# Kernel tuning notes

Hardware: AMD Instinct MI355X
Metric: run time of the kernel (lower is better)

## Reference

```python
import jax, jax.numpy as jnp
import numpy as np

B = 512
V = 6890   # SMPL vertices
NJ = 24    # joints (global)
NB = 10    # shape betas
NP = 207   # pose blendshape features = 23*9
NJO = 19   # cocoplus output joints
PARENTS = np.array([0,0,0,0,1,2,3,4,5,6,7,8,9,9,9,12,13,14,16,17,18,19,20,21], dtype=np.int32)


def setup_inputs() -> dict:
    key = jax.random.key(0)
    ks = jax.random.split(key, 7)
    inputs = jax.random.normal(ks[0], (B, 82), jnp.float32) * 0.2  # [pose(72) | shape(10)]
    v_template = jax.random.normal(ks[1], (V, 3), jnp.float32)
    shapes = jax.random.normal(ks[2], (NB, V * 3), jnp.float32) * 0.01
    posedirs = jax.random.normal(ks[3], (NP, V * 3), jnp.float32) * 0.01
    jr = jax.random.uniform(ks[4], (V, NJ), jnp.float32)
    smpl_regressor = jr / jnp.sum(jr, axis=0, keepdims=True)          # columns sum to 1 over vertices
    w = jax.random.uniform(ks[5], (V, NJ), jnp.float32) ** 4
    lbs_weights = w / jnp.sum(w, axis=1, keepdims=True)               # rows sum to 1 over joints
    cr = jax.random.uniform(ks[6], (V, NJO), jnp.float32)
    joint_regressor = cr / jnp.sum(cr, axis=0, keepdims=True)
    parents = jnp.asarray(PARENTS)
    return {"inputs": inputs, "v_template": v_template, "shapes": shapes,
            "posedirs": posedirs, "smpl_regressor": smpl_regressor,
            "lbs_weights": lbs_weights, "joint_regressor": joint_regressor,
            "parents": parents}


def _rodrigues(pose):  # [B,72] -> [B,24,3,3]
    r = pose.reshape(-1, 3)
    angle = jnp.linalg.norm(r + 1e-8, axis=1, keepdims=True)  # [N,1]
    n = r / angle
    c = jnp.cos(angle)[:, :, None]   # [N,1,1]
    s = jnp.sin(angle)[:, :, None]
    outer = n[:, :, None] * n[:, None, :]
    z = jnp.zeros_like(n[:, 0])
    K = jnp.stack([z, -n[:, 2], n[:, 1],
                   n[:, 2], z, -n[:, 0],
                   -n[:, 1], n[:, 0], z], axis=1).reshape(-1, 3, 3)
    R = c * jnp.eye(3, dtype=pose.dtype) + (1.0 - c) * outer + s * K
    return R.reshape(-1, NJ, 3, 3)


def _make_A(R, t):  # R [B,3,3], t [B,3] -> [B,4,4]
    top = jnp.concatenate([R, t[:, :, None]], axis=2)
    bottom = jnp.broadcast_to(jnp.array([0., 0., 0., 1.], dtype=R.dtype), (R.shape[0], 1, 4))
    return jnp.concatenate([top, bottom], axis=1)


def _global_rigid(rotations, joints, parents_np):
    # sequential kinematic-chain composition over the fixed 24-joint tree
    res = [_make_A(rotations[:, 0], joints[:, 0])]
    for i in range(1, NJ):
        p = int(parents_np[i])
        t = joints[:, i] - joints[:, p]
        res.append(jnp.matmul(res[p], _make_A(rotations[:, i], t)))
    A_world = jnp.stack(res, axis=1)                 # [B,24,4,4]
    new_J = A_world[:, :, :3, 3]
    Jw0 = jnp.concatenate([joints, jnp.zeros(joints.shape[:2] + (1,), joints.dtype)], axis=2)[..., None]
    init_bone = jnp.matmul(A_world, Jw0)[..., 0]     # [B,24,4]
    pad = jnp.zeros_like(A_world).at[:, :, :, 3].set(init_bone)
    return new_J, A_world - pad


def reference(inputs, v_template, shapes, posedirs, smpl_regressor, lbs_weights, joint_regressor, parents):
    b = inputs.shape[0]
    pose = inputs[:, :72]
    beta = inputs[:, -10:]
    v_shaped = jnp.matmul(beta, shapes).reshape(b, V, 3) + v_template
    v_joints = jnp.einsum('bvc,vj->bjc', v_shaped, smpl_regressor)        # [B,24,3]
    rot = _rodrigues(pose)                                                # [B,24,3,3]
    pose_feature = (rot[:, 1:] - jnp.eye(3, dtype=rot.dtype)).reshape(b, -1)  # [B,207]
    v_posed = jnp.matmul(pose_feature, posedirs).reshape(b, V, 3) + v_shaped
    joint_transformed, A = _global_rigid(rot, v_joints, np.asarray(parents))
    T = jnp.einsum('vj,bjk->bvk', lbs_weights, A.reshape(b, NJ, 16)).reshape(b, V, 4, 4)
    v_homo = jnp.concatenate([v_posed, jnp.ones((b, V, 1), v_posed.dtype)], axis=2)
    vertices = jnp.einsum('bvij,bvj->bvi', T, v_homo)[:, :, :3]
    joints = jnp.einsum('bvc,vj->bjc', vertices, joint_regressor)         # [B,19,3]
    return vertices, joints, rot
```

## Files before the change

kernel.cpp:

```cpp
#include <hip/hip_runtime.h>

#define B_   512
#define V_   6890
#define NJ_  24
#define NB_  10
#define NP_  207
#define NJO_ 19



#define SRB_   192
#define SRCH_  862
#define RODB_  48
#define TRB_   26

__global__ void __launch_bounds__(256) k_pre(const float* __restrict__ in,
                                             const float* __restrict__ shapes,
                                             const float* __restrict__ vt,
                                             const float* __restrict__ sreg,
                                             const float* __restrict__ jreg,
                                             float* __restrict__ srtr,
                                             float* __restrict__ out_rot,
                                             float* __restrict__ pf_t,
                                             float* __restrict__ jreg_t,
                                             float* __restrict__ jout) {
  int blk = blockIdx.x;
  int tid = threadIdx.x;
  if (blk < SRB_) {
    int j  = blk >> 3;
    int ch = blk & 7;
    int vend = (ch + 1) * SRCH_; if (vend > V_) vend = V_;
    float acc[33];
#pragma unroll
    for (int a = 0; a < 33; a++) acc[a] = 0.f;
    for (int v = ch * SRCH_ + tid; v < vend; v += 256) {
      float w = sreg[v * NJ_ + j];
#pragma unroll
      for (int k = 0; k < NB_; k++) {
        const float* sp = shapes + k * (V_ * 3) + 3 * v;
#pragma unroll
        for (int c = 0; c < 3; c++) acc[k * 3 + c] += w * sp[c];
      }
#pragma unroll
      for (int c = 0; c < 3; c++) acc[30 + c] += w * vt[3 * v + c];
    }
    __shared__ float red[4][33];
    int wave = tid >> 6, lane = tid & 63;
#pragma unroll
    for (int a = 0; a < 33; a++) {
      float x = acc[a];
#pragma unroll
      for (int m = 1; m < 64; m <<= 1) x += __shfl_xor(x, m, 64);
      if (lane == 0) red[wave][a] = x;
    }
    __syncthreads();
    if (tid < 33) {
      float s = red[0][tid] + red[1][tid] + red[2][tid] + red[3][tid];
      if (tid < 30) atomicAdd(&srtr[((tid / 3) * NJ_ + j) * 3 + (tid % 3)], s);
      else          atomicAdd(&srtr[720 + j * 3 + (tid - 30)], s);
    }
  } else if (blk < SRB_ + RODB_) {
    int idx = (blk - SRB_) * 256 + tid;
    int b = idx & (B_ - 1);
    int j = idx >> 9;
    const float* r = in + b * 82 + j * 3;
    float r0 = r[0], r1 = r[1], r2 = r[2];
    float ax = r0 + 1e-8f, ay = r1 + 1e-8f, az = r2 + 1e-8f;
    float angle = sqrtf(ax * ax + ay * ay + az * az);
    float inv = 1.0f / angle;
    float n0 = r0 * inv, n1 = r1 * inv, n2 = r2 * inv;
    float c = cosf(angle), s = sinf(angle);
    float ic = 1.0f - c;
    float R[9];
    R[0] = c + ic * n0 * n0;      R[1] = ic * n0 * n1 - s * n2;  R[2] = ic * n0 * n2 + s * n1;
    R[3] = ic * n1 * n0 + s * n2; R[4] = c + ic * n1 * n1;       R[5] = ic * n1 * n2 - s * n0;
    R[6] = ic * n2 * n0 - s * n1; R[7] = ic * n2 * n1 + s * n0;  R[8] = c + ic * n2 * n2;
    float* ro = out_rot + b * 216 + j * 9;
#pragma unroll
    for (int q = 0; q < 9; q++) ro[q] = R[q];
    if (j > 0) {
#pragma unroll
      for (int q = 0; q < 9; q++)
        pf_t[(size_t)((j - 1) * 9 + q) * B_ + b] = R[q] - ((q % 4 == 0) ? 1.0f : 0.0f);
    }
  } else {
    int idx = (blk - SRB_ - RODB_) * 256 + tid;
    for (int q = idx; q < B_ * NJO_ * 3; q += TRB_ * 256) jout[q] = 0.f;
    if (idx < B_) pf_t[(size_t)NP_ * B_ + idx] = 0.f;
    for (int e = idx; e < V_ * NJO_; e += TRB_ * 256) {
      int jo = e / V_;
      int v  = e - jo * V_;
      jreg_t[e] = jreg[v * NJO_ + jo];
    }
  }
}

__global__ void __launch_bounds__(192) k_chain(const float* __restrict__ in,
                                               const float* __restrict__ rot,
                                               const float* __restrict__ srtr,
                                               const int* __restrict__ parents,
                                               float* __restrict__ Abuf) {
  (void)parents;
  constexpr int P[NJ_] = {0, 0, 0, 0, 1, 2, 3, 4, 5, 6, 7, 8, 9, 9, 9, 12, 13, 14,
                          16, 17, 18, 19, 20, 21};
  int tid = threadIdx.x;
  int bl = tid & 63;
  int r  = tid >> 6;
  int b  = blockIdx.x * 64 + bl;
  float beta[NB_];
#pragma unroll
  for (int k = 0; k < NB_; k++) beta[k] = in[b * 82 + 72 + k];
  float J[NJ_][3];
#pragma unroll
  for (int j = 0; j < NJ_; j++) {
#pragma unroll
    for (int c = 0; c < 3; c++) {
      float s = srtr[720 + j * 3 + c];
#pragma unroll
      for (int k = 0; k < NB_; k++) s += beta[k] * srtr[(k * NJ_ + j) * 3 + c];
      J[j][c] = s;
    }
  }
  const float* Rb = rot + b * 216;
  float A[NJ_][4];
#pragma unroll
  for (int c = 0; c < 3; c++) A[0][c] = Rb[r * 3 + c];
  A[0][3] = J[0][r];
#pragma unroll
  for (int j = 1; j < NJ_; j++) {
    const int p = P[j];
    float t0 = J[j][0] - J[p][0];
    float t1 = J[j][1] - J[p][1];
    float t2 = J[j][2] - J[p][2];
    float Rj[9];
#pragma unroll
    for (int q = 0; q < 9; q++) Rj[q] = Rb[j * 9 + q];
    float p0 = A[p][0], p1 = A[p][1], p2 = A[p][2], p3 = A[p][3];
#pragma unroll
    for (int c = 0; c < 3; c++)
      A[j][c] = p0 * Rj[c] + p1 * Rj[3 + c] + p2 * Rj[6 + c];
    A[j][3] = p0 * t0 + p1 * t1 + p2 * t2 + p3;
  }
  float* Ab = Abuf + (size_t)b * 288 + r * 4;
#pragma unroll
  for (int j = 0; j < NJ_; j++) {
    float4 o;
    o.x = A[j][0]; o.y = A[j][1]; o.z = A[j][2];
    o.w = A[j][3] - (A[j][0] * J[j][0] + A[j][1] * J[j][1] + A[j][2] * J[j][2]);
    *reinterpret_cast<float4*>(Ab + j * 12) = o;
  }
}

#define PB_   8
#define BT_   32
#define GX_   108
#define GY_   16
#define NWG_  (GX_ * GY_)
#define TILE_ 8
#define NT_   26
#define ROWF_ 192
__global__ void __launch_bounds__(256) k_main(const float* __restrict__ in,
                                              const float* __restrict__ shapes,
                                              const float* __restrict__ vt,
                                              const float* __restrict__ posedirs,
                                              const float* __restrict__ lbs,
                                              const float* __restrict__ pf_t,
                                              const float* __restrict__ Abuf,
                                              float* __restrict__ verts) {
  __shared__ float lbs_l[64 * 25];
  __shared__ float pd[2][TILE_ * ROWF_];
  int tid = threadIdx.x;
  int raw  = blockIdx.y * GX_ + blockIdx.x;
  int virt = (raw & 7) * (NWG_ / 8) + (raw >> 3);
  int vblk = virt >> 4;
  int bblk = virt & (GY_ - 1);
  int v0 = vblk * 64;
  int b0 = bblk * BT_;
  int nv = V_ - v0; if (nv > 64) nv = 64;
  for (int i = tid; i < nv * NJ_; i += 256)
    lbs_l[(i / NJ_) * 25 + (i % NJ_)] = lbs[(size_t)v0 * NJ_ + i];
  int lane = tid & 63;
  int g = tid >> 6;
  int bb0 = __builtin_amdgcn_readfirstlane(b0 + g * PB_);
  int v = v0 + lane;
  int vc = v < V_ ? v : V_ - 1;

  int srow[6], scol[6];
#pragma unroll
  for (int q = 0; q < 6; q++) {
    int idx = q * 256 + tid;
    srow[q] = idx / ROWF_;
    scol[q] = idx - srow[q] * ROWF_;
  }
  int ebase = 3 * v0;

  float acc[PB_][3];
  {
    float t0 = vt[3 * vc + 0], t1 = vt[3 * vc + 1], t2 = vt[3 * vc + 2];
#pragma unroll
    for (int i = 0; i < PB_; i++) { acc[i][0] = t0; acc[i][1] = t1; acc[i][2] = t2; }
  }
#pragma unroll
  for (int k = 0; k < NB_; k++) {
    const float* sp = shapes + k * (V_ * 3) + 3 * vc;
    float s0 = sp[0], s1 = sp[1], s2 = sp[2];
#pragma unroll
    for (int i = 0; i < PB_; i++) {
      float bv = in[(size_t)(bb0 + i) * 82 + 72 + k];
      acc[i][0] += bv * s0; acc[i][1] += bv * s1; acc[i][2] += bv * s2;
    }
  }
  {
    float stg[6];
#pragma unroll
    for (int q = 0; q < 6; q++) {
      int rg = srow[q];
      int off = ebase + scol[q]; if (off > V_ * 3 - 1) off = V_ * 3 - 1;
      stg[q] = posedirs[(size_t)rg * (V_ * 3) + off];
    }
    __syncthreads();
#pragma unroll
    for (int q = 0; q < 6; q++) pd[0][q * 256 + tid] = stg[q];
    __syncthreads();
  }
  for (int t = 0; t < NT_; t++) {
    float stg[6];
    const bool more = (t + 1 < NT_);
    if (more) {
#pragma unroll
      for (int q = 0; q < 6; q++) {
        int rg = (t + 1) * TILE_ + srow[q]; if (rg > NP_ - 1) rg = NP_ - 1;
        int off = ebase + scol[q]; if (off > V_ * 3 - 1) off = V_ * 3 - 1;
        stg[q] = posedirs[(size_t)rg * (V_ * 3) + off];
      }
    }
    const float* pdb = pd[t & 1];
#pragma unroll
    for (int r = 0; r < TILE_; r++) {
      float d0 = pdb[r * ROWF_ + 3 * lane + 0];
      float d1 = pdb[r * ROWF_ + 3 * lane + 1];
      float d2 = pdb[r * ROWF_ + 3 * lane + 2];
      const float* pfp = pf_t + (size_t)(t * TILE_ + r) * B_ + bb0;
#pragma unroll
      for (int i = 0; i < PB_; i++) {
        float f = pfp[i];
        acc[i][0] += f * d0; acc[i][1] += f * d1; acc[i][2] += f * d2;
      }
    }
    if (more) {
      float* dst = pd[(t + 1) & 1];
#pragma unroll
      for (int q = 0; q < 6; q++) dst[q * 256 + tid] = stg[q];
    }
    __syncthreads();
  }
  float o[PB_][3];
#pragma unroll
  for (int i = 0; i < PB_; i++) { o[i][0] = 0.f; o[i][1] = 0.f; o[i][2] = 0.f; }
  for (int j = 0; j < NJ_; j++) {
    float w = lbs_l[lane * 25 + j];
#pragma unroll
    for (int i = 0; i < PB_; i++) {
      const float* M = Abuf + (size_t)(bb0 + i) * 288 + j * 12;
      float x = acc[i][0], y = acc[i][1], z = acc[i][2];
      o[i][0] += w * (M[0] * x + M[1] * y + M[2]  * z + M[3]);
      o[i][1] += w * (M[4] * x + M[5] * y + M[6]  * z + M[7]);
      o[i][2] += w * (M[8] * x + M[9] * y + M[10] * z + M[11]);
    }
  }
  if (v < V_) {
#pragma unroll
    for (int i = 0; i < PB_; i++) {
      float* op = verts + (size_t)(bb0 + i) * (V_ * 3) + 3 * v;
      op[0] = o[i][0]; op[1] = o[i][1]; op[2] = o[i][2];
    }
  }
}

#define JCH_ 1728
__global__ void __launch_bounds__(256) k_joints(const float* __restrict__ verts,
                                                const float* __restrict__ jreg_t,
                                                float* __restrict__ jout) {
  int b = blockIdx.x;
  int ch = blockIdx.y;
  int tid = threadIdx.x;
  int vend = (ch + 1) * JCH_; if (vend > V_) vend = V_;
  float acc[NJO_ * 3];
#pragma unroll
  for (int a = 0; a < NJO_ * 3; a++) acc[a] = 0.f;
  const float* vb = verts + (size_t)b * V_ * 3;
  for (int v = ch * JCH_ + tid; v < vend; v += 256) {
    float x = vb[3 * v + 0], y = vb[3 * v + 1], z = vb[3 * v + 2];
#pragma unroll
    for (int jo = 0; jo < NJO_; jo++) {
      float w = jreg_t[jo * V_ + v];
      acc[jo * 3 + 0] += w * x; acc[jo * 3 + 1] += w * y; acc[jo * 3 + 2] += w * z;
    }
  }
  __shared__ float red[4][NJO_ * 3];
  int wave = tid >> 6, lane = tid & 63;
#pragma unroll
  for (int a = 0; a < NJO_ * 3; a++) {
    float x = acc[a];
#pragma unroll
    for (int m = 1; m < 64; m <<= 1) x += __shfl_xor(x, m, 64);
    if (lane == 0) red[wave][a] = x;
  }
  __syncthreads();
  if (tid < NJO_ * 3) {
    float s = red[0][tid] + red[1][tid] + red[2][tid] + red[3][tid];
    atomicAdd(&jout[b * (NJO_ * 3) + tid], s);
  }
}

extern "C" void kernel_launch(void* const* d_in, const int* in_sizes, int n_in,
                              void* d_out, int out_size, void* d_ws, size_t ws_size,
                              hipStream_t stream) {
  const float* inputs   = (const float*)d_in[0];
  const float* v_templ  = (const float*)d_in[1];
  const float* shapes   = (const float*)d_in[2];
  const float* posedirs = (const float*)d_in[3];
  const float* sreg     = (const float*)d_in[4];
  const float* lbs      = (const float*)d_in[5];
  const float* jreg     = (const float*)d_in[6];
  const int*   parents  = (const int*)d_in[7];

  float* out   = (float*)d_out;
  float* verts = out;
  float* jout  = out + 10583040;
  float* rot   = out + 10612224;

  float* ws     = (float*)d_ws;
  float* pf_t   = ws;
  float* Abuf   = ws + 106496;
  float* srtr   = ws + 106496 + 147456;
  float* jreg_t = srtr + 792;

  hipMemsetAsync(srtr, 0, 792 * sizeof(float), stream);

  k_pre  <<<SRB_ + RODB_ + TRB_, 256, 0, stream>>>(inputs, shapes, v_templ, sreg, jreg,
                                                   srtr, rot, pf_t, jreg_t, jout);
  k_chain<<<8, 192, 0, stream>>>(inputs, rot, srtr, parents, Abuf);
  dim3 gmain(GX_, GY_);
  k_main <<<gmain, 256, 0, stream>>>(inputs, shapes, v_templ, posedirs, lbs, pf_t, Abuf, verts);
  dim3 gj(B_, 4);
  k_joints<<<gj, 256, 0, stream>>>(verts, jreg_t, jout);
}
```

Before: 287.3 us.

## Fold shape blendshapes into posedirs tiled loop and stage pose features in LDS

The shape-blendshape accumulation becomes part of the same double-buffered tiled K loop as the pose blendshapes. Shape rows and posedirs rows are concatenated into 217 rows, with the trip count raised from 26 to 28. The per-batch coefficients (betas or pose features) are now staged cooperatively into shared memory each tile and read as float4, instead of each wave doing scalar global loads. This aims to cut redundant global/scalar coefficient loads and the separate shape pass. It adds one extra tile of work and some branching in the staging loads.

Result: slower. 304.3 us (+5.9%).

```diff
diff --git a/kernel.cpp b/kernel.cpp
--- a/kernel.cpp
+++ b/kernel.cpp
@@ -2,6 +2,7 @@
 
 #define B_   512
 #define V_   6890
+#define V3_  20670
 #define NJ_  24
 #define NB_  10
 #define NP_  207
@@ -37,7 +38,7 @@
       float w = sreg[v * NJ_ + j];
 #pragma unroll
       for (int k = 0; k < NB_; k++) {
-        const float* sp = shapes + k * (V_ * 3) + 3 * v;
+        const float* sp = shapes + k * V3_ + 3 * v;
 #pragma unroll
         for (int c = 0; c < 3; c++) acc[k * 3 + c] += w * sp[c];
       }
@@ -86,7 +87,6 @@
   } else {
     int idx = (blk - SRB_ - RODB_) * 256 + tid;
     for (int q = idx; q < B_ * NJO_ * 3; q += TRB_ * 256) jout[q] = 0.f;
-    if (idx < B_) pf_t[(size_t)NP_ * B_ + idx] = 0.f;
     for (int e = idx; e < V_ * NJO_; e += TRB_ * 256) {
       int jo = e / V_;
       int v  = e - jo * V_;
@@ -157,7 +157,7 @@
 #define GY_   16
 #define NWG_  (GX_ * GY_)
 #define TILE_ 8
-#define NT_   26
+#define NT_   28
 #define ROWF_ 192
 __global__ void __launch_bounds__(256) k_main(const float* __restrict__ in,
                                               const float* __restrict__ shapes,
@@ -169,6 +169,7 @@
                                               float* __restrict__ verts) {
   __shared__ float lbs_l[64 * 25];
   __shared__ float pd[2][TILE_ * ROWF_];
+  __shared__ float pf_l[2][TILE_][32];
   int tid = threadIdx.x;
   int raw  = blockIdx.y * GX_ + blockIdx.x;
   int virt = (raw & 7) * (NWG_ / 8) + (raw >> 3);
@@ -193,6 +194,8 @@
     scol[q] = idx - srow[q] * ROWF_;
   }
   int ebase = 3 * v0;
+  int prow = tid >> 5;
+  int pcol = tid & 31;
 
   float acc[PB_][3];
   {
@@ -200,39 +203,36 @@
 #pragma unroll
     for (int i = 0; i < PB_; i++) { acc[i][0] = t0; acc[i][1] = t1; acc[i][2] = t2; }
   }
-#pragma unroll
-  for (int k = 0; k < NB_; k++) {
-    const float* sp = shapes + k * (V_ * 3) + 3 * vc;
-    float s0 = sp[0], s1 = sp[1], s2 = sp[2];
-#pragma unroll
-    for (int i = 0; i < PB_; i++) {
-      float bv = in[(size_t)(bb0 + i) * 82 + 72 + k];
-      acc[i][0] += bv * s0; acc[i][1] += bv * s1; acc[i][2] += bv * s2;
-    }
-  }
   {
     float stg[6];
 #pragma unroll
     for (int q = 0; q < 6; q++) {
-      int rg = srow[q];
-      int off = ebase + scol[q]; if (off > V_ * 3 - 1) off = V_ * 3 - 1;
-      stg[q] = posedirs[(size_t)rg * (V_ * 3) + off];
-    }
+      int off = ebase + scol[q]; if (off > V3_ - 1) off = V3_ - 1;
+      stg[q] = shapes[(size_t)srow[q] * V3_ + off];
+    }
+    float pfs = in[(size_t)(b0 + pcol) * 82 + 72 + prow];
     __syncthreads();
 #pragma unroll
     for (int q = 0; q < 6; q++) pd[0][q * 256 + tid] = stg[q];
+    pf_l[0][prow][pcol] = pfs;
     __syncthreads();
   }
   for (int t = 0; t < NT_; t++) {
-    float stg[6];
+    float stg[6], pfs;
     const bool more = (t + 1 < NT_);
     if (more) {
 #pragma unroll
       for (int q = 0; q < 6; q++) {
-        int rg = (t + 1) * TILE_ + srow[q]; if (rg > NP_ - 1) rg = NP_ - 1;
-        int off = ebase + scol[q]; if (off > V_ * 3 - 1) off = V_ * 3 - 1;
-        stg[q] = posedirs[(size_t)rg * (V_ * 3) + off];
+        int rg = (t + 1) * TILE_ + srow[q]; if (rg > 216) rg = 216;
+        const float* src = (rg < NB_) ? (shapes + (size_t)rg * V3_)
+                                      : (posedirs + (size_t)(rg - NB_) * V3_);
+        int off = ebase + scol[q]; if (off > V3_ - 1) off = V3_ - 1;
+        stg[q] = src[off];
       }
+      int rgf = (t + 1) * TILE_ + prow;
+      if (rgf < NB_)      pfs = in[(size_t)(b0 + pcol) * 82 + 72 + rgf];
+      else if (rgf < 217) pfs = pf_t[(size_t)(rgf - NB_) * B_ + b0 + pcol];
+      else                pfs = 0.f;
     }
     const float* pdb = pd[t & 1];
 #pragma unroll
@@ -240,17 +240,22 @@
       float d0 = pdb[r * ROWF_ + 3 * lane + 0];
       float d1 = pdb[r * ROWF_ + 3 * lane + 1];
       float d2 = pdb[r * ROWF_ + 3 * lane + 2];
-      const float* pfp = pf_t + (size_t)(t * TILE_ + r) * B_ + bb0;
-#pragma unroll
-      for (int i = 0; i < PB_; i++) {
-        float f = pfp[i];
-        acc[i][0] += f * d0; acc[i][1] += f * d1; acc[i][2] += f * d2;
-      }
+      const float4 fA = *reinterpret_cast<const float4*>(&pf_l[t & 1][r][g * 8]);
+      const float4 fB = *reinterpret_cast<const float4*>(&pf_l[t & 1][r][g * 8 + 4]);
+      acc[0][0] += fA.x * d0; acc[0][1] += fA.x * d1; acc[0][2] += fA.x * d2;
+      acc[1][0] += fA.y * d0; acc[1][1] += fA.y * d1; acc[1][2] += fA.y * d2;
+      acc[2][0] += fA.z * d0; acc[2][1] += fA.z * d1; acc[2][2] += fA.z * d2;
+      acc[3][0] += fA.w * d0; acc[3][1] += fA.w * d1; acc[3][2] += fA.w * d2;
+      acc[4][0] += fB.x * d0; acc[4][1] += fB.x * d1; acc[4][2] += fB.x * d2;
+      acc[5][0] += fB.y * d0; acc[5][1] += fB.y * d1; acc[5][2] += fB.y * d2;
+      acc[6][0] += fB.z * d0; acc[6][1] += fB.z * d1; acc[6][2] += fB.z * d2;
+      acc[7][0] += fB.w * d0; acc[7][1] += fB.w * d1; acc[7][2] += fB.w * d2;
     }
     if (more) {
       float* dst = pd[(t + 1) & 1];
 #pragma unroll
       for (int q = 0; q < 6; q++) dst[q * 256 + tid] = stg[q];
+      pf_l[(t + 1) & 1][prow][pcol] = pfs;
     }
     __syncthreads();
   }
@@ -332,8 +337,8 @@
 
   float* ws     = (float*)d_ws;
   float* pf_t   = ws;
-  float* Abuf   = ws + 106496;
-  float* srtr   = ws + 106496 + 147456;
+  float* Abuf   = ws + 105984;
+  float* srtr   = ws + 105984 + 147456;
   float* jreg_t = srtr + 792;
 
   hipMemsetAsync(srtr, 0, 792 * sizeof(float), stream);
```
